# Kernel tuning notes

Measured on AMD Instinct MI355X. Metric: run time of the kernel, lower is better.

The kernel has to match this reference:

```python
import jax, jax.numpy as jnp
import numpy as np

S, N_SUB, E_SUB = 64, 1024, 16384       # subgraphs, nodes/subgraph, edges/subgraph
N, E = 65536, 1048576                   # global nodes / edges
F_IN, NHID, NCLS, HEADS = 128, 128, 64, 2
RATIO = 0.5
K = int(np.ceil(RATIO * N_SUB))         # SAGPooling keeps K=512 nodes


def setup_inputs() -> dict:
    key = jax.random.key(0)
    ks = jax.random.split(key, 12)
    def lin(k, i, o):
        return jax.random.normal(k, (i, o), jnp.float32) / np.sqrt(i).astype(np.float32)
    return {
        'sub_x': jax.random.normal(ks[0], (S, N_SUB, F_IN), jnp.float32),
        'sub_edge_index': jax.random.randint(ks[1], (S, 2, E_SUB), 0, N_SUB, jnp.int32),
        'sub_orig_idx': jax.random.randint(ks[2], (S, N_SUB), 0, N, jnp.int32),
        'edge_index': jax.random.randint(ks[3], (2, E), 0, N, jnp.int32),
        'W1': lin(ks[4], F_IN, NHID), 'b1': jnp.zeros((NHID,), jnp.float32),
        'W2': lin(ks[5], NHID, NHID), 'b2': jnp.zeros((NHID,), jnp.float32),
        'Wp': lin(ks[6], NHID, 1), 'bp': jnp.zeros((1,), jnp.float32),
        'Wsc': lin(ks[7], NHID, NHID), 'bsc': jnp.zeros((NHID,), jnp.float32),
        'Wqkv': lin(ks[8], 2 * NHID, 6 * NHID), 'bqkv': jnp.zeros((6 * NHID,), jnp.float32),
        'Wo': lin(ks[9], 2 * NHID, 2 * NHID), 'bo': jnp.zeros((2 * NHID,), jnp.float32),
        'Wf': lin(ks[10], 3 * NHID, NCLS), 'bf': jnp.zeros((NCLS,), jnp.float32),
    }


def gcn(x, src, dst, ew, W, b, n):
    """PyG GCNConv: sym-normalized aggregation with self-loops; ew masks invalid edges."""
    h = x @ W
    deg = jax.ops.segment_sum(ew, dst, num_segments=n) + 1.0  # +1 self-loop
    dinv = jax.lax.rsqrt(deg)
    coef = dinv[src] * dinv[dst] * ew
    agg = jax.ops.segment_sum(h[src] * coef[:, None], dst, num_segments=n)
    return agg + h * (dinv * dinv)[:, None] + b


def _forward(sub_x, W1, b1, W2, b2, Wp, bp, Wsc, bsc, Wqkv, bqkv, Wo, bo, Wf, bf,
             sub_edge_index, sub_orig_idx, edge_index):
    dt = sub_x.dtype

    def cacos(x, ei):  # one subgraph: [N_SUB,F], [2,E_SUB]
        src, dst = ei[0], ei[1]
        ew1 = jnp.ones((E_SUB,), dt)
        x1 = jax.nn.relu(gcn(x, src, dst, ew1, W1, b1, N_SUB))
        x2 = jax.nn.relu(gcn(x1, src, dst, ew1, W2, b2, N_SUB))
        # SAGPooling on x1: GCN scorer -> top-k -> tanh gate
        score = gcn(x1, src, dst, ew1, Wp, bp, N_SUB)[:, 0]
        top_s, perm = jax.lax.top_k(score, K)
        x_pool = x1[perm] * jnp.tanh(top_s)[:, None]
        # remap edges to pooled indexing; invalid edges get weight 0
        pos = jnp.full((N_SUB,), -1, jnp.int32).at[perm].set(jnp.arange(K, dtype=jnp.int32))
        valid = (pos[src] >= 0) & (pos[dst] >= 0)
        psrc = jnp.where(valid, pos[src], 0)
        pdst = jnp.where(valid, pos[dst], 0)
        ew2 = valid.astype(dt)
        emb1 = jnp.concatenate([x_pool.max(0), x_pool.mean(0)])  # [2*NHID]
        x_sub = jax.nn.relu(gcn(x_pool, psrc, pdst, ew2, Wsc, bsc, K))
        emb2 = jnp.concatenate([x_sub.max(0), x_sub.mean(0)])
        return x2, emb1 + emb2

    node_embs, sub_embs = jax.vmap(cacos)(sub_x, sub_edge_index)  # [S,N_SUB,NHID], [S,2*NHID]

    # multi-head self-attention over subgraph embeddings (seq_len = 1 per the torch reshape)
    HD = (2 * NHID) // HEADS
    qkv = (sub_embs @ Wqkv + bqkv).reshape(S, 1, 3, HEADS, HD).transpose(2, 0, 3, 1, 4)
    q, k, v = qkv[0], qkv[1], qkv[2]                      # [S,H,1,HD]
    attn = jax.nn.softmax(jnp.einsum('shqd,shkd->shqk', q, k) / np.sqrt(HD).astype(np.float32), axis=-1)
    o = jnp.einsum('shqk,shkd->shqd', attn, v).transpose(0, 2, 1, 3).reshape(S, 1, 2 * NHID)
    att = (o @ Wo + bo)[:, 0]                             # [S, 2*NHID]

    # scatter-add per-node embeddings + broadcast subgraph embedding into global buffer
    combined = jnp.concatenate(
        [node_embs, jnp.broadcast_to(att[:, None, :], (S, N_SUB, 2 * NHID))], axis=-1)
    global_emb = jnp.zeros((N, 3 * NHID), dt).at[sub_orig_idx.reshape(-1)].add(
        combined.reshape(-1, 3 * NHID))

    logits = gcn(global_emb, edge_index[0], edge_index[1], jnp.ones((E,), dt), Wf, bf, N)
    return jax.nn.log_softmax(logits, axis=-1), global_emb


def reference(sub_x, sub_edge_index, sub_orig_idx, edge_index, W1, b1, W2, b2, Wp, bp,
              Wsc, bsc, Wqkv, bqkv, Wo, bo, Wf, bf):
    return _forward(sub_x, W1, b1, W2, b2, Wp, bp, Wsc, bsc, Wqkv, bqkv, Wo, bo, Wf, bf,
                    sub_edge_index, sub_orig_idx, edge_index)
```

## Files before the change

kernel.cpp:

```cpp
#include <hip/hip_runtime.h>
#include <math.h>

#define S     64
#define NSUB  1024
#define ESUB  16384
#define NG    65536
#define EG    1048576
#define NH    128
#define KSEL  512
#define BCAP  20480

__global__ __launch_bounds__(1024) void k_csr_sub(const int* __restrict__ sei,
        const int* __restrict__ sorig, int* __restrict__ rowptr, int* __restrict__ col,
        float* __restrict__ dinv, int* __restrict__ cntR) {
    int b = blockIdx.x, t = threadIdx.x;
    if (b >= 64) {
        int r = (b - 64) * 1024 + t;
        atomicAdd(&cntR[sorig[r]], 1);
        return;
    }
    __shared__ int sh[1024];
    __shared__ int curL[1024];
    int s = b;
    curL[t] = 0;
    __syncthreads();
    const int* dstp = sei + s * 2 * ESUB + ESUB;
    #pragma unroll
    for (int k = 0; k < 16; k++) atomicAdd(&curL[dstp[k * 1024 + t]], 1);
    __syncthreads();
    int v = curL[t];
    sh[t] = v;
    __syncthreads();
    for (int off = 1; off < 1024; off <<= 1) {
        int add = (t >= off) ? sh[t - off] : 0;
        __syncthreads();
        sh[t] += add;
        __syncthreads();
    }
    int incl = sh[t];
    int excl = incl - v;
    rowptr[s * (NSUB + 1) + t] = excl;
    dinv[s * NSUB + t] = rsqrtf((float)(v + 1));
    if (t == 1023) rowptr[s * (NSUB + 1) + NSUB] = incl;
    curL[t] = s * ESUB + excl;
    __syncthreads();
    const int* srcp = sei + s * 2 * ESUB;
    #pragma unroll
    for (int k = 0; k < 16; k++) {
        int e = k * 1024 + t;
        int src = srcp[e];
        int dst = dstp[e];
        int p = atomicAdd(&curL[dst], 1);
        col[p] = src;
    }
}

template<int KDIM, int NCOL>
__global__ __launch_bounds__(256) void k_matmul(const float* __restrict__ X,
        const float* __restrict__ W, float* __restrict__ Y) {
    __shared__ float As[16][72];
    __shared__ float Bs[16][72];
    int t = threadIdx.x;
    int row0 = blockIdx.x * 64;
    int col0 = blockIdx.y * 64;
    int tr = t >> 4, tc = t & 15;
    float acc[4][4] = {};
    for (int k0 = 0; k0 < KDIM; k0 += 16) {
        {
            int r = t >> 2, kq = t & 3;
            float4 v = *(const float4*)&X[(size_t)(row0 + r) * KDIM + k0 + kq * 4];
            As[kq * 4 + 0][r] = v.x; As[kq * 4 + 1][r] = v.y;
            As[kq * 4 + 2][r] = v.z; As[kq * 4 + 3][r] = v.w;
        }
        {
            int k = t >> 4, cq = t & 15;
            float4 v = *(const float4*)&W[(size_t)(k0 + k) * NCOL + col0 + cq * 4];
            *(float4*)&Bs[k][cq * 4] = v;
        }
        __syncthreads();
        #pragma unroll
        for (int k = 0; k < 16; k++) {
            float a0 = As[k][tr * 4 + 0], a1 = As[k][tr * 4 + 1];
            float a2 = As[k][tr * 4 + 2], a3 = As[k][tr * 4 + 3];
            float b0 = Bs[k][tc * 4 + 0], b1 = Bs[k][tc * 4 + 1];
            float b2 = Bs[k][tc * 4 + 2], b3 = Bs[k][tc * 4 + 3];
            acc[0][0] += a0 * b0; acc[0][1] += a0 * b1; acc[0][2] += a0 * b2; acc[0][3] += a0 * b3;
            acc[1][0] += a1 * b0; acc[1][1] += a1 * b1; acc[1][2] += a1 * b2; acc[1][3] += a1 * b3;
            acc[2][0] += a2 * b0; acc[2][1] += a2 * b1; acc[2][2] += a2 * b2; acc[2][3] += a2 * b3;
            acc[3][0] += a3 * b0; acc[3][1] += a3 * b1; acc[3][2] += a3 * b2; acc[3][3] += a3 * b3;
        }
        __syncthreads();
    }
    #pragma unroll
    for (int i = 0; i < 4; i++) {
        float4 v = { acc[i][0], acc[i][1], acc[i][2], acc[i][3] };
        *(float4*)&Y[(size_t)(row0 + tr * 4 + i) * NCOL + col0 + tc * 4] = v;
    }
}

template<bool SCORE>
__global__ __launch_bounds__(256) void k_agg128(const float4* __restrict__ h,
        const float* __restrict__ dinv, const int* __restrict__ rowptr,
        const int* __restrict__ col, const float* __restrict__ bias,
        const float* __restrict__ Wp, float4* __restrict__ out,
        float* __restrict__ scoreh) {
    int b = blockIdx.x;
    int s = b & 63;
    int chunk = b >> 6;
    int t = threadIdx.x;
    int nl = chunk * 8 + (t >> 5);
    int f4 = t & 31;
    const int* rp = rowptr + s * (NSUB + 1);
    int st = rp[nl], en = rp[nl + 1];
    const int* cl = col + s * ESUB;
    const float* dv = dinv + s * NSUB;
    float4 acc = {0.f, 0.f, 0.f, 0.f};
    for (int p = st; p < en; p++) {
        int src = cl[p];
        float d = dv[src];
        float4 hv = h[((size_t)(s * NSUB + src)) * 32 + f4];
        acc.x += hv.x * d; acc.y += hv.y * d; acc.z += hv.z * d; acc.w += hv.w * d;
    }
    size_t node = (size_t)s * NSUB + nl;
    float dn = dv[nl];
    float dn2 = dn * dn;
    float4 hs = h[node * 32 + f4];
    float4 bb = ((const float4*)bias)[f4];
    float4 r;
    r.x = fmaxf(acc.x * dn + hs.x * dn2 + bb.x, 0.f);
    r.y = fmaxf(acc.y * dn + hs.y * dn2 + bb.y, 0.f);
    r.z = fmaxf(acc.z * dn + hs.z * dn2 + bb.z, 0.f);
    r.w = fmaxf(acc.w * dn + hs.w * dn2 + bb.w, 0.f);
    out[node * 32 + f4] = r;
    if (SCORE) {
        float4 wp = ((const float4*)Wp)[f4];
        float p = r.x * wp.x + r.y * wp.y + r.z * wp.z + r.w * wp.w;
        #pragma unroll
        for (int o = 16; o > 0; o >>= 1) p += __shfl_xor(p, o, 32);
        if (f4 == 0) scoreh[node] = p;
    }
}

__global__ void k_score_agg(const float* __restrict__ sh, const float* __restrict__ dinv,
                            const int* __restrict__ rowptr, const int* __restrict__ col,
                            const float* __restrict__ bp, float* __restrict__ score) {
    int n = blockIdx.x * 256 + threadIdx.x;
    int s = n >> 10, nl = n & (NSUB - 1);
    const int* rp = rowptr + s * (NSUB + 1);
    const int* cl = col + s * ESUB;
    const float* dv = dinv + s * NSUB;
    int st = rp[nl], en = rp[nl + 1];
    float acc = 0.f;
    for (int p = st; p < en; p++) {
        int src = cl[p];
        acc += sh[s * NSUB + src] * dv[src];
    }
    float dn = dv[nl];
    score[n] = acc * dn + sh[n] * dn * dn + bp[0];
}

__global__ __launch_bounds__(512) void k_topk(const float* __restrict__ score,
        int* __restrict__ perm, float* __restrict__ gate, int* __restrict__ posmap) {
    __shared__ float sv[1024];
    __shared__ int   si[1024];
    int s = blockIdx.x, t = threadIdx.x;
    for (int i = t; i < 1024; i += 512) {
        sv[i] = score[s * NSUB + i];
        si[i] = i;
        posmap[s * NSUB + i] = -1;
    }
    __syncthreads();
    for (int k = 2; k <= 1024; k <<= 1) {
        for (int j = k >> 1; j > 0; j >>= 1) {
            for (int b = t; b < 1024; b += 512) {
                int ixj = b ^ j;
                if (ixj > b) {
                    bool desc = ((b & k) == 0);
                    bool sw = desc ? (sv[b] < sv[ixj]) : (sv[b] > sv[ixj]);
                    if (sw) {
                        float tv = sv[b]; sv[b] = sv[ixj]; sv[ixj] = tv;
                        int ti = si[b]; si[b] = si[ixj]; si[ixj] = ti;
                    }
                }
            }
            __syncthreads();
        }
    }
    if (t < KSEL) {
        perm[s * KSEL + t] = si[t];
        gate[s * KSEL + t] = tanhf(sv[t]);
        posmap[s * NSUB + si[t]] = t;
    }
}

__global__ __launch_bounds__(256) void k_pool(const float4* __restrict__ x1,
        const int* __restrict__ perm, const float* __restrict__ gate,
        const int* __restrict__ posmap, const int* __restrict__ rowptr,
        const int* __restrict__ col, float* __restrict__ dinv2,
        float4* __restrict__ xpool) {
    int t = threadIdx.x;
    int i = blockIdx.x * 8 + (t >> 5);
    int lane = t & 31;
    int s = i >> 9;
    int n = perm[i];
    const int* rp = rowptr + s * (NSUB + 1);
    const int* cl = col + s * ESUB;
    int st = rp[n], en = rp[n + 1];
    int c = 0;
    for (int p = st + lane; p < en; p += 32) c += (posmap[s * NSUB + cl[p]] >= 0) ? 1 : 0;
    #pragma unroll
    for (int o = 16; o > 0; o >>= 1) c += __shfl_xor(c, o, 32);
    if (lane == 0) dinv2[i] = rsqrtf((float)(c + 1));
    float g = gate[i];
    float4 v = x1[((size_t)(s * NSUB + n)) * 32 + lane];
    v.x *= g; v.y *= g; v.z *= g; v.w *= g;
    xpool[(size_t)i * 32 + lane] = v;
}

__global__ __launch_bounds__(1024) void k_emb(const float* __restrict__ X,
        float* __restrict__ out) {
    __shared__ float red[4][256];
    int s = blockIdx.x, t = threadIdx.x;
    int sl = t >> 8, f = t & 255;
    const float* base = X + (size_t)s * KSEL * NH;
    float r;
    if (f < NH) {
        r = -INFINITY;
        for (int i = sl * 128; i < sl * 128 + 128; i++) r = fmaxf(r, base[i * NH + f]);
    } else {
        r = 0.f;
        for (int i = sl * 128; i < sl * 128 + 128; i++) r += base[i * NH + (f - NH)];
    }
    red[sl][f] = r;
    __syncthreads();
    if (sl == 0) {
        float a = red[0][f], b = red[1][f], c = red[2][f], d = red[3][f];
        float v = (f < NH) ? fmaxf(fmaxf(a, b), fmaxf(c, d)) : (a + b + c + d) * (1.f / KSEL);
        out[s * 256 + f] = v;
    }
}

__global__ __launch_bounds__(1024) void k_emb_attn(const float* __restrict__ X,
        const float* __restrict__ subemb, const float* __restrict__ Wqkv,
        const float* __restrict__ bqkv, const float* __restrict__ Wo,
        const float* __restrict__ bo, const float* __restrict__ Wf,
        float* __restrict__ att, float* __restrict__ AW) {
    __shared__ float red[4][256];
    __shared__ float se[256], t1[256], av[256];
    int s = blockIdx.x, t = threadIdx.x;
    int sl = t >> 8, f = t & 255;
    const float* base = X + (size_t)s * KSEL * NH;
    float r;
    if (f < NH) {
        r = -INFINITY;
        for (int i = sl * 128; i < sl * 128 + 128; i++) r = fmaxf(r, base[i * NH + f]);
    } else {
        r = 0.f;
        for (int i = sl * 128; i < sl * 128 + 128; i++) r += base[i * NH + (f - NH)];
    }
    red[sl][f] = r;
    __syncthreads();
    if (sl == 0) {
        float a = red[0][f], b = red[1][f], c = red[2][f], d = red[3][f];
        float v = (f < NH) ? fmaxf(fmaxf(a, b), fmaxf(c, d)) : (a + b + c + d) * (1.f / KSEL);
        se[f] = subemb[s * 256 + f] + v;
    }
    __syncthreads();
    if (sl == 0) {
        float acc = bqkv[512 + f];
        for (int k = 0; k < 256; k++) acc += se[k] * Wqkv[(size_t)k * 768 + 512 + f];
        t1[f] = acc;
    }
    __syncthreads();
    if (sl == 0) {
        float a2 = bo[f];
        for (int k = 0; k < 256; k++) a2 += t1[k] * Wo[(size_t)k * 256 + f];
        att[s * 256 + f] = a2;
        av[f] = a2;
    }
    __syncthreads();
    if (sl == 0 && f < 64) {
        float acc = 0.f;
        for (int k = 0; k < 256; k++) acc += av[k] * Wf[(size_t)(NH + k) * 64 + f];
        AW[s * 64 + f] = acc;
    }
}

__global__ __launch_bounds__(256) void k_agg_pool(const float4* __restrict__ hp,
        const float* __restrict__ dinv2, const int* __restrict__ perm,
        const int* __restrict__ posmap, const int* __restrict__ rowptr,
        const int* __restrict__ col, const float* __restrict__ bsc,
        float4* __restrict__ xsub) {
    int b = blockIdx.x;
    int s = b & 63;
    int chunk = b >> 6;
    int t = threadIdx.x;
    int il = chunk * 8 + (t >> 5);
    int f4 = t & 31;
    int i = s * KSEL + il;
    int n = perm[i];
    const int* rp = rowptr + s * (NSUB + 1);
    const int* cl = col + s * ESUB;
    int st = rp[n], en = rp[n + 1];
    float4 acc = {0.f, 0.f, 0.f, 0.f};
    for (int p = st; p < en; p++) {
        int j = posmap[s * NSUB + cl[p]];
        if (j >= 0) {
            float d = dinv2[s * KSEL + j];
            float4 hv = hp[((size_t)(s * KSEL + j)) * 32 + f4];
            acc.x += hv.x * d; acc.y += hv.y * d; acc.z += hv.z * d; acc.w += hv.w * d;
        }
    }
    float dn = dinv2[i];
    float dn2 = dn * dn;
    float4 hs = hp[(size_t)i * 32 + f4];
    float4 bb = ((const float4*)bsc)[f4];
    float4 r;
    r.x = fmaxf(acc.x * dn + hs.x * dn2 + bb.x, 0.f);
    r.y = fmaxf(acc.y * dn + hs.y * dn2 + bb.y, 0.f);
    r.z = fmaxf(acc.z * dn + hs.z * dn2 + bb.z, 0.f);
    r.w = fmaxf(acc.w * dn + hs.w * dn2 + bb.w, 0.f);
    xsub[(size_t)i * 32 + f4] = r;
}

__global__ __launch_bounds__(1024) void k_scanN_p1(const int* __restrict__ cnt,
        int* __restrict__ rowptr, float* __restrict__ dscr, int* __restrict__ bsum) {
    __shared__ int sh[1024];
    int b = blockIdx.x, t = threadIdx.x;
    int v = cnt[b * 1024 + t];
    sh[t] = v;
    __syncthreads();
    for (int off = 1; off < 1024; off <<= 1) {
        int add = (t >= off) ? sh[t - off] : 0;
        __syncthreads();
        sh[t] += add;
        __syncthreads();
    }
    int incl = sh[t];
    rowptr[b * 1024 + t] = incl - v;
    dscr[b * 1024 + t] = rsqrtf((float)(v + 1));
    if (t == 1023) bsum[b] = incl;
}

__global__ __launch_bounds__(1024) void k_scanN_p3(int* __restrict__ rowptr,
        int* __restrict__ cur, const int* __restrict__ bsum, int total) {
    __shared__ int sboff;
    int b = blockIdx.x, t = threadIdx.x;
    if (t == 0) {
        int run = 0;
        for (int i = 0; i < b; i++) run += bsum[i];
        sboff = run;
    }
    __syncthreads();
    int idx = b * 1024 + t;
    int r = rowptr[idx] + sboff;
    rowptr[idx] = r;
    cur[idx] = r;
    if (idx == 0) rowptr[NG] = total;
}

__global__ void k_fillR(const int* __restrict__ orig, int* __restrict__ cur,
                        int* __restrict__ rowlist, int* __restrict__ bcur) {
    if (blockIdx.x == 0 && threadIdx.x < 64) bcur[threadIdx.x] = threadIdx.x * BCAP;
    int r = blockIdx.x * 256 + threadIdx.x;
    int p = atomicAdd(&cur[orig[r]], 1);
    rowlist[p] = r;
}

__global__ __launch_bounds__(384) void k_gather(const float4* __restrict__ x2,
        const float4* __restrict__ att, const int* __restrict__ rowptrR,
        const int* __restrict__ rowlist, float4* __restrict__ gemb) {
    int t = threadIdx.x;
    int g = blockIdx.x * 4 + (t / 96);
    int lane = t % 96;
    int st = rowptrR[g], en = rowptrR[g + 1];
    float4 acc = {0.f, 0.f, 0.f, 0.f};
    for (int p = st; p < en; p++) {
        int row = rowlist[p];
        float4 v = (lane < 32) ? x2[(size_t)row * 32 + lane]
                               : att[(size_t)(row >> 10) * 64 + (lane - 32)];
        acc.x += v.x; acc.y += v.y; acc.z += v.z; acc.w += v.w;
    }
    gemb[(size_t)g * 96 + lane] = acc;
}

__global__ __launch_bounds__(256) void k_gatherH(const float4* __restrict__ X2W,
        const float4* __restrict__ AW, const int* __restrict__ rowptrR,
        const int* __restrict__ rowlist, float4* __restrict__ hf) {
    int t = threadIdx.x;
    int g = blockIdx.x * 16 + (t >> 4);
    int f4 = t & 15;
    int st = rowptrR[g], en = rowptrR[g + 1];
    float4 acc = {0.f, 0.f, 0.f, 0.f};
    for (int p = st; p < en; p++) {
        int row = rowlist[p];
        float4 a = X2W[(size_t)row * 16 + f4];
        float4 b = AW[(size_t)(row >> 10) * 16 + f4];
        acc.x += a.x + b.x; acc.y += a.y + b.y; acc.z += a.z + b.z; acc.w += a.w + b.w;
    }
    hf[(size_t)g * 16 + f4] = acc;
}

__global__ __launch_bounds__(256) void k_binN(const int* __restrict__ gei,
        int* __restrict__ bcur, int* __restrict__ ebin) {
    __shared__ int lh[64];
    __shared__ int lbase[64];
    int t = threadIdx.x;
    if (t < 64) lh[t] = 0;
    __syncthreads();
    int e0 = blockIdx.x * 8192;
    #pragma unroll 8
    for (int k = 0; k < 32; k++) {
        int d = gei[EG + e0 + k * 256 + t];
        atomicAdd(&lh[d >> 10], 1);
    }
    __syncthreads();
    if (t < 64) {
        lbase[t] = atomicAdd(&bcur[t], lh[t]);
        lh[t] = 0;
    }
    __syncthreads();
    #pragma unroll 4
    for (int k = 0; k < 32; k++) {
        int idx = e0 + k * 256 + t;
        int d = gei[EG + idx];
        int src = gei[idx];
        int bb = d >> 10;
        int pos = lbase[bb] + atomicAdd(&lh[bb], 1);
        ebin[pos] = src | ((d & 1023) << 16);
    }
}

__global__ __launch_bounds__(1024) void k_fillB3(const int* __restrict__ ebin,
        const int* __restrict__ bcur, int* __restrict__ rowptrN,
        float* __restrict__ dinvN, int* __restrict__ colN) {
    __shared__ int sh[1024];
    __shared__ int curL[1024];
    __shared__ int sbase;
    int b = blockIdx.x, t = threadIdx.x;
    if (t == 0) {
        int run = 0;
        for (int i = 0; i < b; i++) run += bcur[i] - i * BCAP;
        sbase = run;
    }
    curL[t] = 0;
    __syncthreads();
    int st = b * BCAP, en = bcur[b];
    for (int i = st + t; i < en; i += 1024) atomicAdd(&curL[ebin[i] >> 16], 1);
    __syncthreads();
    int v = curL[t];
    sh[t] = v;
    __syncthreads();
    for (int off = 1; off < 1024; off <<= 1) {
        int add = (t >= off) ? sh[t - off] : 0;
        __syncthreads();
        sh[t] += add;
        __syncthreads();
    }
    int incl = sh[t];
    int excl = incl - v;
    int base = sbase;
    rowptrN[(b << 10) + t] = base + excl;
    dinvN[(b << 10) + t] = rsqrtf((float)(v + 1));
    if (b == 63 && t == 1023) rowptrN[NG] = base + incl;
    curL[t] = base + excl;
    __syncthreads();
    for (int i = st + t; i < en; i += 1024) {
        int packed = ebin[i];
        int p = atomicAdd(&curL[packed >> 16], 1);
        colN[p] = packed & 0xFFFF;
    }
}

__global__ __launch_bounds__(256) void k_final(const float4* __restrict__ hf,
        const float* __restrict__ dinvN, const int* __restrict__ rowptr,
        const int* __restrict__ col, const float* __restrict__ bfb,
        float4* __restrict__ out) {
    int t = threadIdx.x;
    int n = blockIdx.x * 16 + (t >> 4);
    int f4 = t & 15;
    int st = rowptr[n], en = rowptr[n + 1];
    float4 acc = {0.f, 0.f, 0.f, 0.f};
    for (int p = st; p < en; p++) {
        int src = col[p];
        float d = dinvN[src];
        float4 hv = hf[(size_t)src * 16 + f4];
        acc.x += hv.x * d; acc.y += hv.y * d; acc.z += hv.z * d; acc.w += hv.w * d;
    }
    float dn = dinvN[n];
    float dn2 = dn * dn;
    float4 hs = hf[(size_t)n * 16 + f4];
    float4 bb = ((const float4*)bfb)[f4];
    float4 x;
    x.x = acc.x * dn + hs.x * dn2 + bb.x;
    x.y = acc.y * dn + hs.y * dn2 + bb.y;
    x.z = acc.z * dn + hs.z * dn2 + bb.z;
    x.w = acc.w * dn + hs.w * dn2 + bb.w;
    float m = fmaxf(fmaxf(x.x, x.y), fmaxf(x.z, x.w));
    for (int o = 1; o < 16; o <<= 1) m = fmaxf(m, __shfl_xor(m, o, 64));
    float ssum = expf(x.x - m) + expf(x.y - m) + expf(x.z - m) + expf(x.w - m);
    for (int o = 1; o < 16; o <<= 1) ssum += __shfl_xor(ssum, o, 64);
    float lz = m + logf(ssum);
    float4 r = { x.x - lz, x.y - lz, x.z - lz, x.w - lz };
    out[(size_t)n * 16 + f4] = r;
}

extern "C" void kernel_launch(void* const* d_in, const int* in_sizes, int n_in,
                              void* d_out, int out_size, void* d_ws, size_t ws_size,
                              hipStream_t stream) {
    const float* sub_x = (const float*)d_in[0];
    const int*   sei   = (const int*)d_in[1];
    const int*   sorig = (const int*)d_in[2];
    const int*   gei   = (const int*)d_in[3];
    const float *W1 = (const float*)d_in[4],  *b1  = (const float*)d_in[5];
    const float *W2 = (const float*)d_in[6],  *b2  = (const float*)d_in[7];
    const float *Wp = (const float*)d_in[8],  *bp  = (const float*)d_in[9];
    const float *Wsc = (const float*)d_in[10], *bsc = (const float*)d_in[11];
    const float *Wqkv = (const float*)d_in[12], *bqkv = (const float*)d_in[13];
    const float *Wo = (const float*)d_in[14], *bo  = (const float*)d_in[15];
    const float *Wf = (const float*)d_in[16], *bfb = (const float*)d_in[17];

    float* out0 = (float*)d_out;
    float* gemb = (float*)d_out + (size_t)NG * 64;

    char* w = (char*)d_ws;
    size_t off = 0;
    auto alloc = [&](size_t nbytes) -> void* {
        off = (off + 255) & ~(size_t)255;
        void* p = w + off;
        off += nbytes;
        return p;
    };
    int*   bsum    = (int*)alloc(64 * 4);
    int*   bcur    = (int*)alloc(64 * 4);
    float* AW      = (float*)alloc((size_t)S * 64 * 4);
    float* dinv    = (float*)alloc((size_t)NG * 4);
    float* scoreh  = (float*)alloc((size_t)NG * 4);
    float* score   = (float*)alloc((size_t)NG * 4);
    float* gate    = (float*)alloc((size_t)S * KSEL * 4);
    float* dinv2   = (float*)alloc((size_t)S * KSEL * 4);
    float* subemb  = (float*)alloc((size_t)S * 256 * 4);
    float* att     = (float*)alloc((size_t)S * 256 * 4);
    int*   perm    = (int*)alloc((size_t)S * KSEL * 4);
    int*   posmap  = (int*)alloc((size_t)NG * 4);
    int*   cur_sub = (int*)alloc((size_t)NG * 4);
    int*   rowptr_s= (int*)alloc((size_t)(NG + 64) * 4);
    int*   col_sub = (int*)alloc((size_t)EG * 4);
    int*   rowptrR = (int*)alloc((size_t)(NG + 64) * 4);
    int*   cntR    = (int*)alloc((size_t)NG * 4);
    int*   rowlist = (int*)alloc((size_t)NG * 4);
    float* x1      = (float*)alloc((size_t)NG * NH * 4);
    float* x2      = (float*)alloc((size_t)NG * NH * 4);
    float* hbuf    = (float*)alloc((size_t)NG * NH * 4);
    float* xpool   = (float*)alloc((size_t)S * KSEL * NH * 4);
    float* xsub    = x1;
    float* hf      = hbuf;
    float* dinvN   = dinv;
    float* X2W     = x1;
    int*   curR    = cur_sub;
    int*   rowptrN = rowptr_s;
    int*   colN    = col_sub;
    int*   ebin    = (int*)xpool;

    hipMemsetAsync(cntR, 0, (size_t)NG * 4, stream);

    k_csr_sub<<<128, 1024, 0, stream>>>(sei, sorig, rowptr_s, col_sub, dinv, cntR);

    k_matmul<128, 128><<<dim3(NG / 64, 2), 256, 0, stream>>>(sub_x, W1, hbuf);
    k_agg128<true><<<8192, 256, 0, stream>>>((const float4*)hbuf, dinv, rowptr_s, col_sub,
                                             b1, Wp, (float4*)x1, scoreh);
    k_matmul<128, 128><<<dim3(NG / 64, 2), 256, 0, stream>>>(x1, W2, hbuf);
    k_agg128<false><<<8192, 256, 0, stream>>>((const float4*)hbuf, dinv, rowptr_s, col_sub,
                                              b2, nullptr, (float4*)x2, nullptr);
    k_score_agg<<<NG / 256, 256, 0, stream>>>(scoreh, dinv, rowptr_s, col_sub, bp, score);
    k_topk<<<S, 512, 0, stream>>>(score, perm, gate, posmap);
    k_pool<<<(S * KSEL) / 8, 256, 0, stream>>>((const float4*)x1, perm, gate, posmap,
                                               rowptr_s, col_sub, dinv2, (float4*)xpool);
    k_emb<<<S, 1024, 0, stream>>>(xpool, subemb);
    k_matmul<128, 128><<<dim3((S * KSEL) / 64, 2), 256, 0, stream>>>(xpool, Wsc, hbuf);
    k_agg_pool<<<4096, 256, 0, stream>>>((const float4*)hbuf, dinv2, perm, posmap,
                                         rowptr_s, col_sub, bsc, (float4*)xsub);
    k_emb_attn<<<S, 1024, 0, stream>>>(xsub, subemb, Wqkv, bqkv, Wo, bo, Wf, att, AW);

    k_scanN_p1<<<64, 1024, 0, stream>>>(cntR, rowptrR, dinv, bsum);
    k_scanN_p3<<<64, 1024, 0, stream>>>(rowptrR, curR, bsum, NG);
    k_fillR<<<NG / 256, 256, 0, stream>>>(sorig, curR, rowlist, bcur);
    k_gather<<<NG / 4, 384, 0, stream>>>((const float4*)x2, (const float4*)att,
                                         rowptrR, rowlist, (float4*)gemb);
    k_matmul<128, 64><<<dim3(NG / 64, 1), 256, 0, stream>>>(x2, Wf, X2W);
    k_gatherH<<<NG / 16, 256, 0, stream>>>((const float4*)X2W, (const float4*)AW,
                                           rowptrR, rowlist, (float4*)hf);

    k_binN<<<EG / 8192, 256, 0, stream>>>(gei, bcur, ebin);
    k_fillB3<<<64, 1024, 0, stream>>>(ebin, bcur, rowptrN, dinvN, colN);

    k_final<<<NG / 16, 256, 0, stream>>>((const float4*)hf, dinvN, rowptrN, colN, bfb, (float4*)out0);

    (void)in_sizes; (void)n_in; (void)out_size; (void)ws_size;
}
```

Before: 717.6 us.

## Merge tail kernels via block-range fusion and enlarge matmul tile to 128x128

The 128-column matmul now uses 128x128 tiles with an 8x8 register block per thread, which gives more reuse per shared-memory load at the cost of higher register pressure and fewer blocks. The two-pass global scan becomes a single kernel in which each block recomputes its prefix offset. Independent tail kernels (row fill plus edge binning, gather plus the Wf matmul, gatherH plus CSR fill) are merged into shared launches by splitting on block index, which reduces launch count and lets independent work run concurrently. The change also stops writing rsqrt values into dinv in the scan; the dinv buffer is aliased as dinvN and filled later, so that write appears to have been redundant.

```diff
diff --git a/kernel.cpp b/kernel.cpp
--- a/kernel.cpp
+++ b/kernel.cpp
@@ -55,46 +55,53 @@
     }
 }
 
-template<int KDIM, int NCOL>
-__global__ __launch_bounds__(256) void k_matmul(const float* __restrict__ X,
+template<int KDIM>
+__global__ __launch_bounds__(256) void k_matmul128(const float* __restrict__ X,
         const float* __restrict__ W, float* __restrict__ Y) {
-    __shared__ float As[16][72];
-    __shared__ float Bs[16][72];
-    int t = threadIdx.x;
-    int row0 = blockIdx.x * 64;
-    int col0 = blockIdx.y * 64;
+    __shared__ float As[16][136];
+    __shared__ float Bs[16][136];
+    int t = threadIdx.x;
+    int row0 = blockIdx.x * 128;
     int tr = t >> 4, tc = t & 15;
-    float acc[4][4] = {};
+    float acc[8][8] = {};
     for (int k0 = 0; k0 < KDIM; k0 += 16) {
         {
-            int r = t >> 2, kq = t & 3;
-            float4 v = *(const float4*)&X[(size_t)(row0 + r) * KDIM + k0 + kq * 4];
-            As[kq * 4 + 0][r] = v.x; As[kq * 4 + 1][r] = v.y;
-            As[kq * 4 + 2][r] = v.z; As[kq * 4 + 3][r] = v.w;
+            int r = t >> 1, half = t & 1;
+            const float* xp = &X[(size_t)(row0 + r) * KDIM + k0 + half * 8];
+            float4 v0 = *(const float4*)xp;
+            float4 v1 = *(const float4*)(xp + 4);
+            int kb = half * 8;
+            As[kb + 0][r] = v0.x; As[kb + 1][r] = v0.y; As[kb + 2][r] = v0.z; As[kb + 3][r] = v0.w;
+            As[kb + 4][r] = v1.x; As[kb + 5][r] = v1.y; As[kb + 6][r] = v1.z; As[kb + 7][r] = v1.w;
         }
         {
-            int k = t >> 4, cq = t & 15;
-            float4 v = *(const float4*)&W[(size_t)(k0 + k) * NCOL + col0 + cq * 4];
-            *(float4*)&Bs[k][cq * 4] = v;
+            int k = t >> 4, c = (t & 15) * 4;
+            *(float4*)&Bs[k][c]      = *(const float4*)&W[(size_t)(k0 + k) * 128 + c];
+            *(float4*)&Bs[k][c + 64] = *(const float4*)&W[(size_t)(k0 + k) * 128 + c + 64];
         }
         __syncthreads();
         #pragma unroll
         for (int k = 0; k < 16; k++) {
-            float a0 = As[k][tr * 4 + 0], a1 = As[k][tr * 4 + 1];
-            float a2 = As[k][tr * 4 + 2], a3 = As[k][tr * 4 + 3];
-            float b0 = Bs[k][tc * 4 + 0], b1 = Bs[k][tc * 4 + 1];
-            float b2 = Bs[k][tc * 4 + 2], b3 = Bs[k][tc * 4 + 3];
-            acc[0][0] += a0 * b0; acc[0][1] += a0 * b1; acc[0][2] += a0 * b2; acc[0][3] += a0 * b3;
-            acc[1][0] += a1 * b0; acc[1][1] += a1 * b1; acc[1][2] += a1 * b2; acc[1][3] += a1 * b3;
-            acc[2][0] += a2 * b0; acc[2][1] += a2 * b1; acc[2][2] += a2 * b2; acc[2][3] += a2 * b3;
-            acc[3][0] += a3 * b0; acc[3][1] += a3 * b1; acc[3][2] += a3 * b2; acc[3][3] += a3 * b3;
+            float a[8], b[8];
+            *(float4*)&a[0] = *(const float4*)&As[k][tr * 8];
+            *(float4*)&a[4] = *(const float4*)&As[k][tr * 8 + 4];
+            *(float4*)&b[0] = *(const float4*)&Bs[k][tc * 8];
+            *(float4*)&b[4] = *(const float4*)&Bs[k][tc * 8 + 4];
+            #pragma unroll
+            for (int i = 0; i < 8; i++)
+                #pragma unroll
+                for (int j = 0; j < 8; j++)
+                    acc[i][j] += a[i] * b[j];
         }
         __syncthreads();
     }
     #pragma unroll
-    for (int i = 0; i < 4; i++) {
-        float4 v = { acc[i][0], acc[i][1], acc[i][2], acc[i][3] };
-        *(float4*)&Y[(size_t)(row0 + tr * 4 + i) * NCOL + col0 + tc * 4] = v;
+    for (int i = 0; i < 8; i++) {
+        float4 v0 = { acc[i][0], acc[i][1], acc[i][2], acc[i][3] };
+        float4 v1 = { acc[i][4], acc[i][5], acc[i][6], acc[i][7] };
+        float* yp = &Y[(size_t)(row0 + tr * 8 + i) * 128 + tc * 8];
+        *(float4*)yp = v0;
+        *(float4*)(yp + 4) = v1;
     }
 }
 
@@ -323,10 +330,25 @@
     xsub[(size_t)i * 32 + f4] = r;
 }
 
-__global__ __launch_bounds__(1024) void k_scanN_p1(const int* __restrict__ cnt,
-        int* __restrict__ rowptr, float* __restrict__ dscr, int* __restrict__ bsum) {
+__global__ __launch_bounds__(1024) void k_scanR(const int* __restrict__ cnt,
+        int* __restrict__ rowptr, int* __restrict__ cur, int* __restrict__ bcur) {
     __shared__ int sh[1024];
+    __shared__ int wsum[16];
+    __shared__ int sboff;
     int b = blockIdx.x, t = threadIdx.x;
+    if (b == 0 && t < 64) bcur[t] = t * BCAP;
+    int pre = 0;
+    for (int i = t; i < b * 1024; i += 1024) pre += cnt[i];
+    #pragma unroll
+    for (int o = 32; o > 0; o >>= 1) pre += __shfl_xor(pre, o, 64);
+    if ((t & 63) == 0) wsum[t >> 6] = pre;
+    __syncthreads();
+    if (t == 0) {
+        int r = 0;
+        #pragma unroll
+        for (int i = 0; i < 16; i++) r += wsum[i];
+        sboff = r;
+    }
     int v = cnt[b * 1024 + t];
     sh[t] = v;
     __syncthreads();
@@ -336,79 +358,29 @@
         sh[t] += add;
         __syncthreads();
     }
-    int incl = sh[t];
-    rowptr[b * 1024 + t] = incl - v;
-    dscr[b * 1024 + t] = rsqrtf((float)(v + 1));
-    if (t == 1023) bsum[b] = incl;
-}
-
-__global__ __launch_bounds__(1024) void k_scanN_p3(int* __restrict__ rowptr,
-        int* __restrict__ cur, const int* __restrict__ bsum, int total) {
-    __shared__ int sboff;
-    int b = blockIdx.x, t = threadIdx.x;
-    if (t == 0) {
-        int run = 0;
-        for (int i = 0; i < b; i++) run += bsum[i];
-        sboff = run;
-    }
-    __syncthreads();
+    int base = sboff;
+    int r = base + sh[t] - v;
     int idx = b * 1024 + t;
-    int r = rowptr[idx] + sboff;
     rowptr[idx] = r;
     cur[idx] = r;
-    if (idx == 0) rowptr[NG] = total;
-}
-
-__global__ void k_fillR(const int* __restrict__ orig, int* __restrict__ cur,
-                        int* __restrict__ rowlist, int* __restrict__ bcur) {
-    if (blockIdx.x == 0 && threadIdx.x < 64) bcur[threadIdx.x] = threadIdx.x * BCAP;
-    int r = blockIdx.x * 256 + threadIdx.x;
-    int p = atomicAdd(&cur[orig[r]], 1);
-    rowlist[p] = r;
-}
-
-__global__ __launch_bounds__(384) void k_gather(const float4* __restrict__ x2,
-        const float4* __restrict__ att, const int* __restrict__ rowptrR,
-        const int* __restrict__ rowlist, float4* __restrict__ gemb) {
-    int t = threadIdx.x;
-    int g = blockIdx.x * 4 + (t / 96);
-    int lane = t % 96;
-    int st = rowptrR[g], en = rowptrR[g + 1];
-    float4 acc = {0.f, 0.f, 0.f, 0.f};
-    for (int p = st; p < en; p++) {
-        int row = rowlist[p];
-        float4 v = (lane < 32) ? x2[(size_t)row * 32 + lane]
-                               : att[(size_t)(row >> 10) * 64 + (lane - 32)];
-        acc.x += v.x; acc.y += v.y; acc.z += v.z; acc.w += v.w;
-    }
-    gemb[(size_t)g * 96 + lane] = acc;
-}
-
-__global__ __launch_bounds__(256) void k_gatherH(const float4* __restrict__ X2W,
-        const float4* __restrict__ AW, const int* __restrict__ rowptrR,
-        const int* __restrict__ rowlist, float4* __restrict__ hf) {
-    int t = threadIdx.x;
-    int g = blockIdx.x * 16 + (t >> 4);
-    int f4 = t & 15;
-    int st = rowptrR[g], en = rowptrR[g + 1];
-    float4 acc = {0.f, 0.f, 0.f, 0.f};
-    for (int p = st; p < en; p++) {
-        int row = rowlist[p];
-        float4 a = X2W[(size_t)row * 16 + f4];
-        float4 b = AW[(size_t)(row >> 10) * 16 + f4];
-        acc.x += a.x + b.x; acc.y += a.y + b.y; acc.z += a.z + b.z; acc.w += a.w + b.w;
-    }
-    hf[(size_t)g * 16 + f4] = acc;
-}
-
-__global__ __launch_bounds__(256) void k_binN(const int* __restrict__ gei,
-        int* __restrict__ bcur, int* __restrict__ ebin) {
+    if (b == 63 && t == 1023) rowptr[NG] = base + sh[t];
+}
+
+__global__ __launch_bounds__(256) void k_fbN(const int* __restrict__ orig,
+        int* __restrict__ cur, int* __restrict__ rowlist,
+        const int* __restrict__ gei, int* __restrict__ bcur, int* __restrict__ ebin) {
+    int t = threadIdx.x;
+    if (blockIdx.x < 256) {
+        int r = blockIdx.x * 256 + t;
+        int p = atomicAdd(&cur[orig[r]], 1);
+        rowlist[p] = r;
+        return;
+    }
     __shared__ int lh[64];
     __shared__ int lbase[64];
-    int t = threadIdx.x;
     if (t < 64) lh[t] = 0;
     __syncthreads();
-    int e0 = blockIdx.x * 8192;
+    int e0 = (blockIdx.x - 256) * 8192;
     #pragma unroll 8
     for (int k = 0; k < 32; k++) {
         int d = gei[EG + e0 + k * 256 + t];
@@ -431,13 +403,94 @@
     }
 }
 
-__global__ __launch_bounds__(1024) void k_fillB3(const int* __restrict__ ebin,
-        const int* __restrict__ bcur, int* __restrict__ rowptrN,
-        float* __restrict__ dinvN, int* __restrict__ colN) {
+__global__ __launch_bounds__(384) void k_gather_x2w(const float4* __restrict__ x2,
+        const float4* __restrict__ att, const int* __restrict__ rowptrR,
+        const int* __restrict__ rowlist, float4* __restrict__ gemb,
+        const float* __restrict__ X, const float* __restrict__ W,
+        float* __restrict__ Y) {
+    int t = threadIdx.x;
+    if (blockIdx.x < NG / 4) {
+        int g = blockIdx.x * 4 + (t / 96);
+        int lane = t % 96;
+        int st = rowptrR[g], en = rowptrR[g + 1];
+        float4 acc = {0.f, 0.f, 0.f, 0.f};
+        for (int p = st; p < en; p++) {
+            int row = rowlist[p];
+            float4 v = (lane < 32) ? x2[(size_t)row * 32 + lane]
+                                   : att[(size_t)(row >> 10) * 64 + (lane - 32)];
+            acc.x += v.x; acc.y += v.y; acc.z += v.z; acc.w += v.w;
+        }
+        gemb[(size_t)g * 96 + lane] = acc;
+        return;
+    }
+    __shared__ float As[16][72];
+    __shared__ float Bs[16][72];
+    int row0 = (blockIdx.x - NG / 4) * 64;
+    int tr = t >> 4, tc = t & 15;
+    float acc[4][4] = {};
+    for (int k0 = 0; k0 < 128; k0 += 16) {
+        if (t < 256) {
+            {
+                int r = t >> 2, kq = t & 3;
+                float4 v = *(const float4*)&X[(size_t)(row0 + r) * 128 + k0 + kq * 4];
+                As[kq * 4 + 0][r] = v.x; As[kq * 4 + 1][r] = v.y;
+                As[kq * 4 + 2][r] = v.z; As[kq * 4 + 3][r] = v.w;
+            }
+            {
+                int k = t >> 4, cq = t & 15;
+                float4 v = *(const float4*)&W[(size_t)(k0 + k) * 64 + cq * 4];
+                *(float4*)&Bs[k][cq * 4] = v;
+            }
+        }
+        __syncthreads();
+        if (t < 256) {
+            #pragma unroll
+            for (int k = 0; k < 16; k++) {
+                float a0 = As[k][tr * 4 + 0], a1 = As[k][tr * 4 + 1];
+                float a2 = As[k][tr * 4 + 2], a3 = As[k][tr * 4 + 3];
+                float b0 = Bs[k][tc * 4 + 0], b1 = Bs[k][tc * 4 + 1];
+                float b2 = Bs[k][tc * 4 + 2], b3 = Bs[k][tc * 4 + 3];
+                acc[0][0] += a0 * b0; acc[0][1] += a0 * b1; acc[0][2] += a0 * b2; acc[0][3] += a0 * b3;
+                acc[1][0] += a1 * b0; acc[1][1] += a1 * b1; acc[1][2] += a1 * b2; acc[1][3] += a1 * b3;
+                acc[2][0] += a2 * b0; acc[2][1] += a2 * b1; acc[2][2] += a2 * b2; acc[2][3] += a2 * b3;
+                acc[3][0] += a3 * b0; acc[3][1] += a3 * b1; acc[3][2] += a3 * b2; acc[3][3] += a3 * b3;
+            }
+        }
+        __syncthreads();
+    }
+    if (t < 256) {
+        #pragma unroll
+        for (int i = 0; i < 4; i++) {
+            float4 v = { acc[i][0], acc[i][1], acc[i][2], acc[i][3] };
+            *(float4*)&Y[(size_t)(row0 + tr * 4 + i) * 64 + tc * 4] = v;
+        }
+    }
+}
+
+__global__ __launch_bounds__(1024) void k_gatherH_fB3(const float4* __restrict__ X2W,
+        const float4* __restrict__ AW, const int* __restrict__ rowptrR,
+        const int* __restrict__ rowlist, float4* __restrict__ hf,
+        const int* __restrict__ ebin, const int* __restrict__ bcur,
+        int* __restrict__ rowptrN, float* __restrict__ dinvN, int* __restrict__ colN) {
+    int t = threadIdx.x;
+    if (blockIdx.x < 1024) {
+        int g = blockIdx.x * 64 + (t >> 4);
+        int f4 = t & 15;
+        int st = rowptrR[g], en = rowptrR[g + 1];
+        float4 acc = {0.f, 0.f, 0.f, 0.f};
+        for (int p = st; p < en; p++) {
+            int row = rowlist[p];
+            float4 a = X2W[(size_t)row * 16 + f4];
+            float4 b = AW[(size_t)(row >> 10) * 16 + f4];
+            acc.x += a.x + b.x; acc.y += a.y + b.y; acc.z += a.z + b.z; acc.w += a.w + b.w;
+        }
+        hf[(size_t)g * 16 + f4] = acc;
+        return;
+    }
     __shared__ int sh[1024];
     __shared__ int curL[1024];
     __shared__ int sbase;
-    int b = blockIdx.x, t = threadIdx.x;
+    int b = blockIdx.x - 1024;
     if (t == 0) {
         int run = 0;
         for (int i = 0; i < b; i++) run += bcur[i] - i * BCAP;
@@ -531,7 +584,6 @@
         off += nbytes;
         return p;
     };
-    int*   bsum    = (int*)alloc(64 * 4);
     int*   bcur    = (int*)alloc(64 * 4);
     float* AW      = (float*)alloc((size_t)S * 64 * 4);
     float* dinv    = (float*)alloc((size_t)NG * 4);
@@ -566,10 +618,10 @@
 
     k_csr_sub<<<128, 1024, 0, stream>>>(sei, sorig, rowptr_s, col_sub, dinv, cntR);
 
-    k_matmul<128, 128><<<dim3(NG / 64, 2), 256, 0, stream>>>(sub_x, W1, hbuf);
+    k_matmul128<128><<<NG / 128, 256, 0, stream>>>(sub_x, W1, hbuf);
     k_agg128<true><<<8192, 256, 0, stream>>>((const float4*)hbuf, dinv, rowptr_s, col_sub,
                                              b1, Wp, (float4*)x1, scoreh);
-    k_matmul<128, 128><<<dim3(NG / 64, 2), 256, 0, stream>>>(x1, W2, hbuf);
+    k_matmul128<128><<<NG / 128, 256, 0, stream>>>(x1, W2, hbuf);
     k_agg128<false><<<8192, 256, 0, stream>>>((const float4*)hbuf, dinv, rowptr_s, col_sub,
                                               b2, nullptr, (float4*)x2, nullptr);
     k_score_agg<<<NG / 256, 256, 0, stream>>>(scoreh, dinv, rowptr_s, col_sub, bp, score);
@@ -577,23 +629,19 @@
     k_pool<<<(S * KSEL) / 8, 256, 0, stream>>>((const float4*)x1, perm, gate, posmap,
                                                rowptr_s, col_sub, dinv2, (float4*)xpool);
     k_emb<<<S, 1024, 0, stream>>>(xpool, subemb);
-    k_matmul<128, 128><<<dim3((S * KSEL) / 64, 2), 256, 0, stream>>>(xpool, Wsc, hbuf);
+    k_matmul128<128><<<(S * KSEL) / 128, 256, 0, stream>>>(xpool, Wsc, hbuf);
     k_agg_pool<<<4096, 256, 0, stream>>>((const float4*)hbuf, dinv2, perm, posmap,
                                          rowptr_s, col_sub, bsc, (float4*)xsub);
     k_emb_attn<<<S, 1024, 0, stream>>>(xsub, subemb, Wqkv, bqkv, Wo, bo, Wf, att, AW);
 
-    k_scanN_p1<<<64, 1024, 0, stream>>>(cntR, rowptrR, dinv, bsum);
-    k_scanN_p3<<<64, 1024, 0, stream>>>(rowptrR, curR, bsum, NG);
-    k_fillR<<<NG / 256, 256, 0, stream>>>(sorig, curR, rowlist, bcur);
-    k_gather<<<NG / 4, 384, 0, stream>>>((const float4*)x2, (const float4*)att,
-                                         rowptrR, rowlist, (float4*)gemb);
-    k_matmul<128, 64><<<dim3(NG / 64, 1), 256, 0, stream>>>(x2, Wf, X2W);
-    k_gatherH<<<NG / 16, 256, 0, stream>>>((const float4*)X2W, (const float4*)AW,
-                                           rowptrR, rowlist, (float4*)hf);
-
-    k_binN<<<EG / 8192, 256, 0, stream>>>(gei, bcur, ebin);
-    k_fillB3<<<64, 1024, 0, stream>>>(ebin, bcur, rowptrN, dinvN, colN);
-
+    k_scanR<<<64, 1024, 0, stream>>>(cntR, rowptrR, curR, bcur);
+    k_fbN<<<384, 256, 0, stream>>>(sorig, curR, rowlist, gei, bcur, ebin);
+    k_gather_x2w<<<NG / 4 + NG / 64, 384, 0, stream>>>((const float4*)x2, (const float4*)att,
+                                                       rowptrR, rowlist, (float4*)gemb,
+                                                       x2, Wf, X2W);
+    k_gatherH_fB3<<<1024 + 64, 1024, 0, stream>>>((const float4*)X2W, (const float4*)AW,
+                                                  rowptrR, rowlist, (float4*)hf,
+                                                  ebin, bcur, rowptrN, dinvN, colN);
     k_final<<<NG / 16, 256, 0, stream>>>((const float4*)hf, dinvN, rowptrN, colN, bfb, (float4*)out0);
 
     (void)in_sizes; (void)n_in; (void)out_size; (void)ws_size;
```

Result: slower. 741.4 us (+3.3%).

## Scatter GCN layer-2 output into reverse-CSR order so global gathers read contiguously

Applied to the files above, without the earlier changes.

The reverse CSR (global node to subgraph rows) is now built right after the subgraph CSR. Its exclusive scan is merged into one kernel in which each block recomputes its prefix offset, and the fill step also records each row's position. The second subgraph aggregation uses that position to write x2 directly in grouped order, so the global-embedding gather and the gatherH pass read consecutive rows instead of indirect ones. The per-subgraph AW term is added in the X2W matmul epilogue rather than inside the gather loop. The cost is an extra index array, a scattered write in the aggregation, and redundant prefix reads in the scan.

```diff
diff --git a/kernel.cpp b/kernel.cpp
--- a/kernel.cpp
+++ b/kernel.cpp
@@ -53,6 +53,50 @@
         int p = atomicAdd(&curL[dst], 1);
         col[p] = src;
     }
+}
+
+__global__ __launch_bounds__(1024) void k_scanR(const int* __restrict__ cnt,
+        int* __restrict__ rowptr, int* __restrict__ cur, int* __restrict__ bcur) {
+    __shared__ int sh[1024];
+    __shared__ int wsum[16];
+    __shared__ int sboff;
+    int b = blockIdx.x, t = threadIdx.x;
+    if (b == 0 && t < 64) bcur[t] = t * BCAP;
+    int pre = 0;
+    for (int i = t; i < b * 1024; i += 1024) pre += cnt[i];
+    #pragma unroll
+    for (int o = 32; o > 0; o >>= 1) pre += __shfl_xor(pre, o, 64);
+    if ((t & 63) == 0) wsum[t >> 6] = pre;
+    __syncthreads();
+    if (t == 0) {
+        int r = 0;
+        #pragma unroll
+        for (int i = 0; i < 16; i++) r += wsum[i];
+        sboff = r;
+    }
+    int v = cnt[b * 1024 + t];
+    sh[t] = v;
+    __syncthreads();
+    for (int off = 1; off < 1024; off <<= 1) {
+        int add = (t >= off) ? sh[t - off] : 0;
+        __syncthreads();
+        sh[t] += add;
+        __syncthreads();
+    }
+    int base = sboff;
+    int r = base + sh[t] - v;
+    int idx = b * 1024 + t;
+    rowptr[idx] = r;
+    cur[idx] = r;
+    if (b == 63 && t == 1023) rowptr[NG] = base + sh[t];
+}
+
+__global__ void k_fillR(const int* __restrict__ orig, int* __restrict__ cur,
+                        int* __restrict__ rowlist, int* __restrict__ posR) {
+    int r = blockIdx.x * 256 + threadIdx.x;
+    int p = atomicAdd(&cur[orig[r]], 1);
+    rowlist[p] = r;
+    posR[r] = p;
 }
 
 template<int KDIM, int NCOL>
@@ -98,12 +142,12 @@
     }
 }
 
-template<bool SCORE>
+template<bool SCORE, bool SCATTER>
 __global__ __launch_bounds__(256) void k_agg128(const float4* __restrict__ h,
         const float* __restrict__ dinv, const int* __restrict__ rowptr,
         const int* __restrict__ col, const float* __restrict__ bias,
-        const float* __restrict__ Wp, float4* __restrict__ out,
-        float* __restrict__ scoreh) {
+        const float* __restrict__ Wp, const int* __restrict__ posR,
+        float4* __restrict__ out, float* __restrict__ scoreh) {
     int b = blockIdx.x;
     int s = b & 63;
     int chunk = b >> 6;
@@ -131,7 +175,8 @@
     r.y = fmaxf(acc.y * dn + hs.y * dn2 + bb.y, 0.f);
     r.z = fmaxf(acc.z * dn + hs.z * dn2 + bb.z, 0.f);
     r.w = fmaxf(acc.w * dn + hs.w * dn2 + bb.w, 0.f);
-    out[node * 32 + f4] = r;
+    size_t orow = SCATTER ? (size_t)posR[node] : node;
+    out[orow * 32 + f4] = r;
     if (SCORE) {
         float4 wp = ((const float4*)Wp)[f4];
         float p = r.x * wp.x + r.y * wp.y + r.z * wp.z + r.w * wp.w;
@@ -323,51 +368,7 @@
     xsub[(size_t)i * 32 + f4] = r;
 }
 
-__global__ __launch_bounds__(1024) void k_scanN_p1(const int* __restrict__ cnt,
-        int* __restrict__ rowptr, float* __restrict__ dscr, int* __restrict__ bsum) {
-    __shared__ int sh[1024];
-    int b = blockIdx.x, t = threadIdx.x;
-    int v = cnt[b * 1024 + t];
-    sh[t] = v;
-    __syncthreads();
-    for (int off = 1; off < 1024; off <<= 1) {
-        int add = (t >= off) ? sh[t - off] : 0;
-        __syncthreads();
-        sh[t] += add;
-        __syncthreads();
-    }
-    int incl = sh[t];
-    rowptr[b * 1024 + t] = incl - v;
-    dscr[b * 1024 + t] = rsqrtf((float)(v + 1));
-    if (t == 1023) bsum[b] = incl;
-}
-
-__global__ __launch_bounds__(1024) void k_scanN_p3(int* __restrict__ rowptr,
-        int* __restrict__ cur, const int* __restrict__ bsum, int total) {
-    __shared__ int sboff;
-    int b = blockIdx.x, t = threadIdx.x;
-    if (t == 0) {
-        int run = 0;
-        for (int i = 0; i < b; i++) run += bsum[i];
-        sboff = run;
-    }
-    __syncthreads();
-    int idx = b * 1024 + t;
-    int r = rowptr[idx] + sboff;
-    rowptr[idx] = r;
-    cur[idx] = r;
-    if (idx == 0) rowptr[NG] = total;
-}
-
-__global__ void k_fillR(const int* __restrict__ orig, int* __restrict__ cur,
-                        int* __restrict__ rowlist, int* __restrict__ bcur) {
-    if (blockIdx.x == 0 && threadIdx.x < 64) bcur[threadIdx.x] = threadIdx.x * BCAP;
-    int r = blockIdx.x * 256 + threadIdx.x;
-    int p = atomicAdd(&cur[orig[r]], 1);
-    rowlist[p] = r;
-}
-
-__global__ __launch_bounds__(384) void k_gather(const float4* __restrict__ x2,
+__global__ __launch_bounds__(384) void k_gather(const float4* __restrict__ x2s,
         const float4* __restrict__ att, const int* __restrict__ rowptrR,
         const int* __restrict__ rowlist, float4* __restrict__ gemb) {
     int t = threadIdx.x;
@@ -375,28 +376,74 @@
     int lane = t % 96;
     int st = rowptrR[g], en = rowptrR[g + 1];
     float4 acc = {0.f, 0.f, 0.f, 0.f};
-    for (int p = st; p < en; p++) {
-        int row = rowlist[p];
-        float4 v = (lane < 32) ? x2[(size_t)row * 32 + lane]
-                               : att[(size_t)(row >> 10) * 64 + (lane - 32)];
-        acc.x += v.x; acc.y += v.y; acc.z += v.z; acc.w += v.w;
+    if (lane < 32) {
+        for (int p = st; p < en; p++) {
+            float4 v = x2s[(size_t)p * 32 + lane];
+            acc.x += v.x; acc.y += v.y; acc.z += v.z; acc.w += v.w;
+        }
+    } else {
+        for (int p = st; p < en; p++) {
+            int sub = rowlist[p] >> 10;
+            float4 v = att[(size_t)sub * 64 + (lane - 32)];
+            acc.x += v.x; acc.y += v.y; acc.z += v.z; acc.w += v.w;
+        }
     }
     gemb[(size_t)g * 96 + lane] = acc;
 }
 
-__global__ __launch_bounds__(256) void k_gatherH(const float4* __restrict__ X2W,
-        const float4* __restrict__ AW, const int* __restrict__ rowptrR,
-        const int* __restrict__ rowlist, float4* __restrict__ hf) {
+__global__ __launch_bounds__(256) void k_x2w(const float* __restrict__ X,
+        const float* __restrict__ W, const int* __restrict__ rowlist,
+        const float* __restrict__ AW, float* __restrict__ Y) {
+    __shared__ float As[16][72];
+    __shared__ float Bs[16][72];
+    int t = threadIdx.x;
+    int row0 = blockIdx.x * 64;
+    int tr = t >> 4, tc = t & 15;
+    float acc[4][4] = {};
+    for (int k0 = 0; k0 < 128; k0 += 16) {
+        {   int r = t >> 2, kq = t & 3;
+            float4 v = *(const float4*)&X[(size_t)(row0 + r) * 128 + k0 + kq * 4];
+            As[kq * 4 + 0][r] = v.x; As[kq * 4 + 1][r] = v.y;
+            As[kq * 4 + 2][r] = v.z; As[kq * 4 + 3][r] = v.w;
+        }
+        {   int k = t >> 4, cq = t & 15;
+            float4 v = *(const float4*)&W[(size_t)(k0 + k) * 64 + cq * 4];
+            *(float4*)&Bs[k][cq * 4] = v;
+        }
+        __syncthreads();
+        #pragma unroll
+        for (int k = 0; k < 16; k++) {
+            float a0 = As[k][tr * 4 + 0], a1 = As[k][tr * 4 + 1];
+            float a2 = As[k][tr * 4 + 2], a3 = As[k][tr * 4 + 3];
+            float b0 = Bs[k][tc * 4 + 0], b1 = Bs[k][tc * 4 + 1];
+            float b2 = Bs[k][tc * 4 + 2], b3 = Bs[k][tc * 4 + 3];
+            acc[0][0] += a0 * b0; acc[0][1] += a0 * b1; acc[0][2] += a0 * b2; acc[0][3] += a0 * b3;
+            acc[1][0] += a1 * b0; acc[1][1] += a1 * b1; acc[1][2] += a1 * b2; acc[1][3] += a1 * b3;
+            acc[2][0] += a2 * b0; acc[2][1] += a2 * b1; acc[2][2] += a2 * b2; acc[2][3] += a2 * b3;
+            acc[3][0] += a3 * b0; acc[3][1] += a3 * b1; acc[3][2] += a3 * b2; acc[3][3] += a3 * b3;
+        }
+        __syncthreads();
+    }
+    #pragma unroll
+    for (int i = 0; i < 4; i++) {
+        int rr = row0 + tr * 4 + i;
+        int sub = rowlist[rr] >> 10;
+        const float4 aw = *(const float4*)&AW[(size_t)sub * 64 + tc * 4];
+        float4 v = { acc[i][0] + aw.x, acc[i][1] + aw.y, acc[i][2] + aw.z, acc[i][3] + aw.w };
+        *(float4*)&Y[(size_t)rr * 64 + tc * 4] = v;
+    }
+}
+
+__global__ __launch_bounds__(256) void k_gatherH(const float4* __restrict__ X2Ws,
+        const int* __restrict__ rowptrR, float4* __restrict__ hf) {
     int t = threadIdx.x;
     int g = blockIdx.x * 16 + (t >> 4);
     int f4 = t & 15;
     int st = rowptrR[g], en = rowptrR[g + 1];
     float4 acc = {0.f, 0.f, 0.f, 0.f};
     for (int p = st; p < en; p++) {
-        int row = rowlist[p];
-        float4 a = X2W[(size_t)row * 16 + f4];
-        float4 b = AW[(size_t)(row >> 10) * 16 + f4];
-        acc.x += a.x + b.x; acc.y += a.y + b.y; acc.z += a.z + b.z; acc.w += a.w + b.w;
+        float4 a = X2Ws[(size_t)p * 16 + f4];
+        acc.x += a.x; acc.y += a.y; acc.z += a.z; acc.w += a.w;
     }
     hf[(size_t)g * 16 + f4] = acc;
 }
@@ -531,7 +578,6 @@
         off += nbytes;
         return p;
     };
-    int*   bsum    = (int*)alloc(64 * 4);
     int*   bcur    = (int*)alloc(64 * 4);
     float* AW      = (float*)alloc((size_t)S * 64 * 4);
     float* dinv    = (float*)alloc((size_t)NG * 4);
@@ -549,14 +595,15 @@
     int*   rowptrR = (int*)alloc((size_t)(NG + 64) * 4);
     int*   cntR    = (int*)alloc((size_t)NG * 4);
     int*   rowlist = (int*)alloc((size_t)NG * 4);
+    int*   posR    = (int*)alloc((size_t)NG * 4);
     float* x1      = (float*)alloc((size_t)NG * NH * 4);
-    float* x2      = (float*)alloc((size_t)NG * NH * 4);
+    float* x2s     = (float*)alloc((size_t)NG * NH * 4);
     float* hbuf    = (float*)alloc((size_t)NG * NH * 4);
     float* xpool   = (float*)alloc((size_t)S * KSEL * NH * 4);
     float* xsub    = x1;
     float* hf      = hbuf;
     float* dinvN   = dinv;
-    float* X2W     = x1;
+    float* X2Ws    = x1;
     int*   curR    = cur_sub;
     int*   rowptrN = rowptr_s;
     int*   colN    = col_sub;
@@ -565,13 +612,15 @@
     hipMemsetAsync(cntR, 0, (size_t)NG * 4, stream);
 
     k_csr_sub<<<128, 1024, 0, stream>>>(sei, sorig, rowptr_s, col_sub, dinv, cntR);
+    k_scanR<<<64, 1024, 0, stream>>>(cntR, rowptrR, curR, bcur);
+    k_fillR<<<NG / 256, 256, 0, stream>>>(sorig, curR, rowlist, posR);
 
     k_matmul<128, 128><<<dim3(NG / 64, 2), 256, 0, stream>>>(sub_x, W1, hbuf);
-    k_agg128<true><<<8192, 256, 0, stream>>>((const float4*)hbuf, dinv, rowptr_s, col_sub,
-                                             b1, Wp, (float4*)x1, scoreh);
+    k_agg128<true, false><<<8192, 256, 0, stream>>>((const float4*)hbuf, dinv, rowptr_s,
+                                                    col_sub, b1, Wp, nullptr, (float4*)x1, scoreh);
     k_matmul<128, 128><<<dim3(NG / 64, 2), 256, 0, stream>>>(x1, W2, hbuf);
-    k_agg128<false><<<8192, 256, 0, stream>>>((const float4*)hbuf, dinv, rowptr_s, col_sub,
-                                              b2, nullptr, (float4*)x2, nullptr);
+    k_agg128<false, true><<<8192, 256, 0, stream>>>((const float4*)hbuf, dinv, rowptr_s,
+                                                    col_sub, b2, nullptr, posR, (float4*)x2s, nullptr);
     k_score_agg<<<NG / 256, 256, 0, stream>>>(scoreh, dinv, rowptr_s, col_sub, bp, score);
     k_topk<<<S, 512, 0, stream>>>(score, perm, gate, posmap);
     k_pool<<<(S * KSEL) / 8, 256, 0, stream>>>((const float4*)x1, perm, gate, posmap,
@@ -582,18 +631,14 @@
                                          rowptr_s, col_sub, bsc, (float4*)xsub);
     k_emb_attn<<<S, 1024, 0, stream>>>(xsub, subemb, Wqkv, bqkv, Wo, bo, Wf, att, AW);
 
-    k_scanN_p1<<<64, 1024, 0, stream>>>(cntR, rowptrR, dinv, bsum);
-    k_scanN_p3<<<64, 1024, 0, stream>>>(rowptrR, curR, bsum, NG);
-    k_fillR<<<NG / 256, 256, 0, stream>>>(sorig, curR, rowlist, bcur);
-    k_gather<<<NG / 4, 384, 0, stream>>>((const float4*)x2, (const float4*)att,
-                                         rowptrR, rowlist, (float4*)gemb);
-    k_matmul<128, 64><<<dim3(NG / 64, 1), 256, 0, stream>>>(x2, Wf, X2W);
-    k_gatherH<<<NG / 16, 256, 0, stream>>>((const float4*)X2W, (const float4*)AW,
-                                           rowptrR, rowlist, (float4*)hf);
-
     k_binN<<<EG / 8192, 256, 0, stream>>>(gei, bcur, ebin);
     k_fillB3<<<64, 1024, 0, stream>>>(ebin, bcur, rowptrN, dinvN, colN);
 
+    k_gather<<<NG / 4, 384, 0, stream>>>((const float4*)x2s, (const float4*)att,
+                                         rowptrR, rowlist, (float4*)gemb);
+    k_x2w<<<NG / 64, 256, 0, stream>>>(x2s, Wf, rowlist, AW, X2Ws);
+    k_gatherH<<<NG / 16, 256, 0, stream>>>((const float4*)X2Ws, rowptrR, (float4*)hf);
+
     k_final<<<NG / 16, 256, 0, stream>>>((const float4*)hf, dinvN, rowptrN, colN, bfb, (float4*)out0);
 
     (void)in_sizes; (void)n_in; (void)out_size; (void)ws_size;
```

Measured after the change: 720.7 us. Within noise of the previous version (+0.4%).
